# Kernel tuning notes

Measured on AMD Instinct MI355X. Metric: run time of the kernel, lower is better.

The kernel has to match this reference:

```python
import jax, jax.numpy as jnp
import numpy as np

B, T, NA, H, C = 64, 128, 2048, 1024, 10  # batch, time, n_act, hidden_units, classes
FORGET_BIAS = 1.0  # tf BasicLSTMCell default


def setup_inputs() -> dict:
    key = jax.random.key(0)
    ks = jax.random.split(key, 5)
    s = 0.02
    return {
        "inputs": jax.random.normal(ks[0], (B, T, NA), jnp.float32),
        "W0": jax.random.normal(ks[1], (NA + H, 4 * H), jnp.float32) * s,
        "b0": jnp.zeros((4 * H,), jnp.float32),
        "W1": jax.random.normal(ks[2], (2 * H, 4 * H), jnp.float32) * s,
        "b1": jnp.zeros((4 * H,), jnp.float32),
        "Wout": jax.random.normal(ks[3], (H, C), jnp.float32) * s,
        "bout": jnp.zeros((C,), jnp.float32),
    }


def _lstm_step(c, h, x, W, b):
    # tf.contrib.rnn.BasicLSTMCell: z = [x; h] @ W + b, gates order i, j, f, o
    z = jnp.concatenate([x, h], axis=-1) @ W + b
    i, j, f, o = jnp.split(z, 4, axis=-1)
    c_new = c * jax.nn.sigmoid(f + FORGET_BIAS) + jax.nn.sigmoid(i) * jnp.tanh(j)
    h_new = jnp.tanh(c_new) * jax.nn.sigmoid(o)
    return c_new, h_new


def reference(inputs, W0, b0, W1, b1, Wout, bout):
    Bz = inputs.shape[0]
    Hd = Wout.shape[0]

    def step(carry, x_t):
        c0, h0, c1, h1 = carry
        c0, h0 = _lstm_step(c0, h0, x_t, W0, b0)   # layer 0
        c1, h1 = _lstm_step(c1, h1, h0, W1, b1)    # layer 1
        return (c0, h0, c1, h1), h1

    z = jnp.zeros((Bz, Hd), inputs.dtype)
    init = (z, z, z, z)  # zero_state for both layers
    xs = jnp.swapaxes(inputs, 0, 1)  # [T, B, NA]
    _, hs = jax.lax.scan(step, init, xs)  # hs: [T, B, H]
    hs = jnp.swapaxes(hs, 0, 1)  # [B, T, H]
    logits = hs @ Wout + bout  # xw_plus_b on flattened outputs
    preds = jax.nn.softmax(logits, axis=-1)  # [B, T, C]
    return preds
```

## Files before the change

kernel.cpp:

```cpp
#include <hip/hip_runtime.h>
#include <stdint.h>


typedef __attribute__((ext_vector_type(4))) float f32x4;
typedef __attribute__((ext_vector_type(8))) short short8x;
typedef unsigned short ushort_t;

constexpr int B_  = 64;
constexpr int T_  = 128;
constexpr int NA_ = 2048;
constexpr int H_  = 1024;
constexpr int C_  = 10;
constexpr int BT_ = B_ * T_;
constexpr int G4_ = 4 * H_;
constexpr int HB_ = B_ * H_;
constexpr int CH_ = 32;
constexpr int MC_ = B_ * CH_;
constexpr int NWG_ = 256;

__device__ __forceinline__ ushort_t f2bf(float x) {
    uint32_t u = __float_as_uint(x);
    uint32_t r = (u + 0x7FFFu + ((u >> 16) & 1u)) >> 16;
    return (ushort_t)r;
}
__device__ __forceinline__ float bf2f(ushort_t h) {
    return __uint_as_float((uint32_t)h << 16);
}
__device__ __forceinline__ float sigmf(float x) { return 1.0f / (1.0f + expf(-x)); }

__device__ __forceinline__ void st_u32(void* p, uint32_t v) {
    __hip_atomic_store((uint32_t*)p, v, __ATOMIC_RELAXED, __HIP_MEMORY_SCOPE_AGENT);
}
__device__ __forceinline__ void st_u64(void* p, uint64_t v) {
    __hip_atomic_store((uint64_t*)p, v, __ATOMIC_RELAXED, __HIP_MEMORY_SCOPE_AGENT);
}

#define AH_ISSUE(dst, ptr) \
    asm volatile("global_load_dwordx4 %0, %1, off sc0 sc1" : "=v"(dst) : "v"(ptr))

#define GLOAD_LDS(gp, lp) \
    __builtin_amdgcn_global_load_lds((const __attribute__((address_space(1))) uint32_t*)(gp), \
                                     (__attribute__((address_space(3))) uint32_t*)(lp), 16, 0, 0)

__global__ void decomp_chunk(const float* __restrict__ X, int c,
                             ushort_t* __restrict__ Hi, ushort_t* __restrict__ Lo) {
    const int i = blockIdx.x * blockDim.x + threadIdx.x;
    if (i >= MC_ * NA_ / 4) return;
    const int mp = i >> 9;
    const int kq = i & 511;
    const int b = mp >> 5, j = mp & 31;
    const size_t src = ((size_t)(b * T_ + c * CH_ + j)) * NA_ + (size_t)kq * 4;
    float4 v = *(const float4*)(X + src);
    ushort4 hi, lo;
    hi.x = f2bf(v.x); lo.x = f2bf(v.x - bf2f(hi.x));
    hi.y = f2bf(v.y); lo.y = f2bf(v.y - bf2f(hi.y));
    hi.z = f2bf(v.z); lo.z = f2bf(v.z - bf2f(hi.z));
    hi.w = f2bf(v.w); lo.w = f2bf(v.w - bf2f(hi.w));
    ((ushort4*)Hi)[i] = hi;
    ((ushort4*)Lo)[i] = lo;
}

__global__ void transdec(const float* __restrict__ W, int rowOff, int Klen,
                         ushort_t* __restrict__ Thi, ushort_t* __restrict__ Tlo,
                         int swz) {
    __shared__ float tile[32][33];
    const int k0 = blockIdx.x * 32, n0 = blockIdx.y * 32;
    const int tx = threadIdx.x & 31, ty = threadIdx.x >> 5;
#pragma unroll
    for (int i = 0; i < 32; i += 8)
        tile[ty + i][tx] = W[(size_t)(rowOff + k0 + ty + i) * G4_ + n0 + tx];
    __syncthreads();
#pragma unroll
    for (int i = 0; i < 32; i += 8) {
        float v = tile[tx][ty + i];
        int n = n0 + ty + i;
        int kk = k0 + tx;
        ushort_t hi = f2bf(v);
        Thi[(size_t)n * Klen + kk] = hi;
        int kl = swz ? (kk ^ ((n & 7) << 3)) : kk;
        Tlo[(size_t)n * Klen + kl] = f2bf(v - bf2f(hi));
    }
}

__global__ __launch_bounds__(256, 2)
void gemm_bf16x3(const ushort_t* __restrict__ Ahi, const ushort_t* __restrict__ Alo,
                 const ushort_t* __restrict__ Bhi, const ushort_t* __restrict__ Blo,
                 float* __restrict__ C, int M, int N, int K) {
    __shared__ ushort_t sA[2][128 * 64];
    __shared__ ushort_t sB[2][128 * 64];

    const int tid  = threadIdx.x;
    const int lane = tid & 63;
    const int wv   = tid >> 6;
    const int wr   = wv >> 1, wc = wv & 1;
    const int tiles_n = N >> 7;
    int id = blockIdx.x;
    const int q8 = gridDim.x >> 3;
    id = (id & 7) * q8 + (id >> 3);
    const int tm = (id / tiles_n) * 128, tn = (id % tiles_n) * 128;

    f32x4 acc[4][4] = {};

    for (int k0 = 0; k0 < K; k0 += 64) {
#pragma unroll
        for (int rd = 0; rd < 4; ++rd) {
            const int off = rd * 4096 + tid * 16;
            const int r   = off >> 7;
            const int kc  = ((off >> 4) & 7) ^ (r & 7);
            const size_t aoff = (size_t)(tm + r) * K + k0 + kc * 8;
            const size_t boff = (size_t)(tn + r) * K + k0 + kc * 8;
            const int dst = (rd * 4096 + wv * 1024) >> 1;
            GLOAD_LDS(Ahi + aoff, (ushort_t*)sA[0] + dst);
            GLOAD_LDS(Alo + aoff, (ushort_t*)sA[1] + dst);
            GLOAD_LDS(Bhi + boff, (ushort_t*)sB[0] + dst);
            GLOAD_LDS(Blo + boff, (ushort_t*)sB[1] + dst);
        }
        __syncthreads();
#pragma unroll
        for (int ks = 0; ks < 2; ++ks) {
            short8x ah[4], al[4], bh[4], bl[4];
#pragma unroll
            for (int i = 0; i < 4; ++i) {
                const int kc = ks * 4 + (lane >> 4);
                const int ra = wr * 64 + i * 16 + (lane & 15);
                const int ea = ra * 64 + ((kc ^ (ra & 7)) * 8);
                ah[i] = *(const short8x*)(&sA[0][ea]);
                al[i] = *(const short8x*)(&sA[1][ea]);
                const int rb = wc * 64 + i * 16 + (lane & 15);
                const int eb = rb * 64 + ((kc ^ (rb & 7)) * 8);
                bh[i] = *(const short8x*)(&sB[0][eb]);
                bl[i] = *(const short8x*)(&sB[1][eb]);
            }
#pragma unroll
            for (int i = 0; i < 4; ++i)
#pragma unroll
                for (int j = 0; j < 4; ++j) {
                    acc[i][j] = __builtin_amdgcn_mfma_f32_16x16x32_bf16(ah[i], bh[j], acc[i][j], 0, 0, 0);
                    acc[i][j] = __builtin_amdgcn_mfma_f32_16x16x32_bf16(ah[i], bl[j], acc[i][j], 0, 0, 0);
                    acc[i][j] = __builtin_amdgcn_mfma_f32_16x16x32_bf16(al[i], bh[j], acc[i][j], 0, 0, 0);
                }
        }
        __syncthreads();
    }
#pragma unroll
    for (int i = 0; i < 4; ++i)
#pragma unroll
        for (int j = 0; j < 4; ++j)
#pragma unroll
            for (int qq = 0; qq < 4; ++qq) {
                const int row = tm + wr * 64 + i * 16 + (lane >> 4) * 4 + qq;
                const int col = tn + wc * 64 + j * 16 + (lane & 15);
                C[(size_t)row * N + col] = acc[i][j][qq];
            }
}

__device__ __forceinline__ void grid_bar(unsigned* slots, unsigned* flag, unsigned epoch) {
    __syncthreads();
    if (threadIdx.x == 0)
        __hip_atomic_store(&slots[blockIdx.x], epoch, __ATOMIC_RELAXED, __HIP_MEMORY_SCOPE_AGENT);
    if (blockIdx.x == 0) {
        if (threadIdx.x < NWG_) {
            unsigned spins = 0;
            while (__hip_atomic_load(&slots[threadIdx.x], __ATOMIC_RELAXED, __HIP_MEMORY_SCOPE_AGENT) < epoch
                   && ++spins < (1u << 20))
                __builtin_amdgcn_s_sleep(4);
        }
        __syncthreads();
        if (threadIdx.x == 0)
            __hip_atomic_store(flag, epoch, __ATOMIC_RELAXED, __HIP_MEMORY_SCOPE_AGENT);
    } else {
        if (threadIdx.x == 0) {
            unsigned spins = 0;
            while (__hip_atomic_load(flag, __ATOMIC_RELAXED, __HIP_MEMORY_SCOPE_AGENT) < epoch
                   && ++spins < (1u << 20))
                __builtin_amdgcn_s_sleep(4);
        }
    }
    __syncthreads();
}

__global__ __launch_bounds__(512, 1)
void lstm_persist(int t0, int t1,
                  const float* __restrict__ Z0c,
                  const ushort_t* __restrict__ W0hT_hi, const ushort_t* __restrict__ W0hT_lo,
                  const ushort_t* __restrict__ W1T_hi,  const ushort_t* __restrict__ W1T_lo,
                  const float* __restrict__ b0, const float* __restrict__ b1,
                  ushort_t* __restrict__ h0hi, ushort_t* __restrict__ h1hi,
                  float* __restrict__ c0, float* __restrict__ c1,
                  ushort_t* __restrict__ hs, unsigned* slots, unsigned* flag) {
    const int w = blockIdx.x;
    const bool isL0 = (w < 128);
    const int u0 = (isL0 ? w : w - 128) * 8;
    const int tid = threadIdx.x, lane = tid & 63, kv = tid >> 6;
    const int K   = isL0 ? H_ : 2 * H_;
    const int KS  = K >> 3;
    const int NKS = KS >> 5;
    const int kbase = kv * KS;

    __shared__ ushort_t slo[32 * 2048];
    __shared__ float zbuf[64][33];

    const ushort_t* Whi = isL0 ? W0hT_hi : W1T_hi;
    const ushort_t* Wlo = isL0 ? W0hT_lo : W1T_lo;

    const int nis = K >> 9;
    for (int g = 0; g < 4; ++g)
        for (int is = 0; is < nis; ++is) {
            const size_t selem = (size_t)(g * H_ + u0) * K + is * 4096 + kv * 512 + (size_t)lane * 8;
            ushort_t* dst = slo + g * 8 * K + is * 4096 + kv * 512;
            GLOAD_LDS(Wlo + selem, dst);
        }
    short8x wh[2][8] = {};
#pragma unroll
    for (int jn = 0; jn < 2; ++jn)
#pragma unroll
        for (int s = 0; s < 8; ++s)
            if (s < NKS) {
                const int n = jn * 16 + (lane & 15);
                const int grow = (n >> 3) * H_ + u0 + (n & 7);
                wh[jn][s] = *(const short8x*)(Whi + (size_t)grow * K + kbase + s * 32 + (lane >> 4) * 8);
            }
    __syncthreads();

    const bool epi = (tid < 256);
    const int em = tid >> 2;
    const int jp = (tid & 3) * 2;
    const int eu = u0 + jp;
    const float* bias = isL0 ? b0 : b1;
    const float bi0 = epi ? bias[eu]            : 0.f, bi1 = epi ? bias[eu + 1]            : 0.f;
    const float bj0 = epi ? bias[H_ + eu]       : 0.f, bj1 = epi ? bias[H_ + eu + 1]       : 0.f;
    const float bf0 = epi ? bias[2 * H_ + eu]   : 0.f, bf1 = epi ? bias[2 * H_ + eu + 1]   : 0.f;
    const float bo0 = epi ? bias[3 * H_ + eu]   : 0.f, bo1 = epi ? bias[3 * H_ + eu + 1]   : 0.f;
    const int zm = tid >> 3, zj = tid & 7;

    for (int t = t0; t < t1; ++t) {
        const bool active = isL0 ? (t < T_) : (t >= 1);
        if (active) {
            const int tt = isL0 ? t : t - 1;
            const ushort_t* Ah;
            int ka0;
            if (isL0)          { Ah = h0hi + ((tt + 1) & 1) * HB_; ka0 = kbase; }
            else if (kv < 4)   { Ah = h0hi + (tt & 1) * HB_;       ka0 = kbase; }
            else               { Ah = h1hi + ((tt + 1) & 1) * HB_; ka0 = kbase - H_; }

            zbuf[zm][zj] = 0.f; zbuf[zm][8 + zj] = 0.f;
            zbuf[zm][16 + zj] = 0.f; zbuf[zm][24 + zj] = 0.f;
            __syncthreads();

            float2 zx0 = {0.f, 0.f}, zx1 = {0.f, 0.f}, zx2 = {0.f, 0.f}, zx3 = {0.f, 0.f};
            if (isL0 && epi) {
                const float* zr = Z0c + ((size_t)em * CH_ + (tt & (CH_ - 1))) * G4_;
                zx0 = *(const float2*)(zr + eu);
                zx1 = *(const float2*)(zr + H_ + eu);
                zx2 = *(const float2*)(zr + 2 * H_ + eu);
                zx3 = *(const float2*)(zr + 3 * H_ + eu);
            }

            f32x4 acc[4][2] = {};
            short8x ah[2][4];
            const int npass = NKS >> 1;
#pragma unroll
            for (int pp = 0; pp < 4; ++pp)
                if (pp < npass) {
#pragma unroll
                    for (int s2 = 0; s2 < 2; ++s2) {
                        const int s = pp * 2 + s2;
                        const int kaa = ka0 + s * 32 + (lane >> 4) * 8;
#pragma unroll
                        for (int i = 0; i < 4; ++i)
                            AH_ISSUE(ah[s2][i], Ah + (size_t)(i * 16 + (lane & 15)) * H_ + kaa);
                    }
                    asm volatile("s_waitcnt vmcnt(0)" ::: "memory");
                    __builtin_amdgcn_sched_barrier(0);
#pragma unroll
                    for (int s2 = 0; s2 < 2; ++s2) {
                        const int s = pp * 2 + s2;
                        const int kw = kbase + s * 32 + (lane >> 4) * 8;
                        const int n0_ = (lane & 15);
                        short8x bl0 = *(const short8x*)(&slo[n0_ * K + (kw ^ ((n0_ & 7) << 3))]);
                        const int n1_ = 16 + (lane & 15);
                        short8x bl1 = *(const short8x*)(&slo[n1_ * K + (kw ^ ((n1_ & 7) << 3))]);
#pragma unroll
                        for (int i = 0; i < 4; ++i) {
                            acc[i][0] = __builtin_amdgcn_mfma_f32_16x16x32_bf16(ah[s2][i], wh[0][s], acc[i][0], 0, 0, 0);
                            acc[i][1] = __builtin_amdgcn_mfma_f32_16x16x32_bf16(ah[s2][i], wh[1][s], acc[i][1], 0, 0, 0);
                            acc[i][0] = __builtin_amdgcn_mfma_f32_16x16x32_bf16(ah[s2][i], bl0, acc[i][0], 0, 0, 0);
                            acc[i][1] = __builtin_amdgcn_mfma_f32_16x16x32_bf16(ah[s2][i], bl1, acc[i][1], 0, 0, 0);
                        }
                    }
                }
#pragma unroll
            for (int i2 = 0; i2 < 4; ++i2) {
                const int i = (i2 + (kv & 3)) & 3;
#pragma unroll
                for (int jn2 = 0; jn2 < 2; ++jn2) {
                    const int jn = (jn2 + (kv >> 2)) & 1;
#pragma unroll
                    for (int qq = 0; qq < 4; ++qq) {
                        const int m = i * 16 + (lane >> 4) * 4 + qq;
                        const int n = jn * 16 + (lane & 15);
                        atomicAdd(&zbuf[m][n], acc[i][jn][qq]);
                    }
                }
            }
            __syncthreads();

            if (epi) {
                const float zi0 = zbuf[em][jp]          + bi0 + zx0.x;
                const float zi1 = zbuf[em][jp + 1]      + bi1 + zx0.y;
                const float zj0 = zbuf[em][8 + jp]      + bj0 + zx1.x;
                const float zj1 = zbuf[em][8 + jp + 1]  + bj1 + zx1.y;
                const float zf0 = zbuf[em][16 + jp]     + bf0 + zx2.x;
                const float zf1 = zbuf[em][16 + jp + 1] + bf1 + zx2.y;
                const float zo0 = zbuf[em][24 + jp]     + bo0 + zx3.x;
                const float zo1 = zbuf[em][24 + jp + 1] + bo1 + zx3.y;
                const size_t sidx = (size_t)em * H_ + eu;
                float* cp = (isL0 ? c0 : c1) + sidx;
                const float cn0 = cp[0] * sigmf(zf0 + 1.0f) + sigmf(zi0) * tanhf(zj0);
                const float cn1 = cp[1] * sigmf(zf1 + 1.0f) + sigmf(zi1) * tanhf(zj1);
                union { float f[2]; uint64_t u; } cu;
                cu.f[0] = cn0; cu.f[1] = cn1;
                st_u64(cp, cu.u);
                const float hv0 = tanhf(cn0) * sigmf(zo0);
                const float hv1 = tanhf(cn1) * sigmf(zo1);
                const uint32_t hhp = (uint32_t)f2bf(hv0) | ((uint32_t)f2bf(hv1) << 16);
                if (isL0) {
                    st_u32(h0hi + (tt & 1) * HB_ + sidx, hhp);
                } else {
                    st_u32(h1hi + (tt & 1) * HB_ + sidx, hhp);
                    st_u32(hs + ((size_t)em * T_ + tt) * H_ + eu, hhp);
                }
            }
        }
        if (t < T_) grid_bar(slots, flag, (unsigned)(t + 1));
    }
}

__global__ __launch_bounds__(256)
void out_softmax(const ushort_t* __restrict__ hs, const float* __restrict__ Wout,
                 const float* __restrict__ bout, float* __restrict__ out) {
    const int row  = blockIdx.x * 4 + (threadIdx.x >> 6);
    const int lane = threadIdx.x & 63;
    const ushort_t* h = hs + (size_t)row * H_;
    float s[C_];
#pragma unroll
    for (int c = 0; c < C_; ++c) s[c] = 0.f;
    for (int k = lane; k < H_; k += 64) {
        const float hv = bf2f(h[k]);
        const float* w = Wout + k * C_;
#pragma unroll
        for (int c = 0; c < C_; ++c) s[c] += hv * w[c];
    }
#pragma unroll
    for (int c = 0; c < C_; ++c) {
#pragma unroll
        for (int d = 32; d > 0; d >>= 1) s[c] += __shfl_xor(s[c], d);
        s[c] += bout[c];
    }
    float mx = s[0];
#pragma unroll
    for (int c = 1; c < C_; ++c) mx = fmaxf(mx, s[c]);
    float sum = 0.f;
#pragma unroll
    for (int c = 0; c < C_; ++c) { s[c] = expf(s[c] - mx); sum += s[c]; }
    const float inv = 1.0f / sum;
    if (lane < C_) {
        float pv = 0.f;
#pragma unroll
        for (int c = 0; c < C_; ++c)
            if (lane == c) pv = s[c] * inv;
        out[(size_t)row * C_ + lane] = pv;
    }
}

extern "C" void kernel_launch(void* const* d_in, const int* in_sizes, int n_in,
                              void* d_out, int out_size, void* d_ws, size_t ws_size,
                              hipStream_t stream) {
    const float* X    = (const float*)d_in[0];
    const float* W0   = (const float*)d_in[1];
    const float* b0   = (const float*)d_in[2];
    const float* W1   = (const float*)d_in[3];
    const float* b1   = (const float*)d_in[4];
    const float* Wout = (const float*)d_in[5];
    const float* bout = (const float*)d_in[6];
    float* out = (float*)d_out;

    char* p = (char*)d_ws;
    size_t off = 0;
    auto take = [&](size_t bytes) { char* r = p + off; off += bytes; return r; };
    ushort_t* W0xT_hi = (ushort_t*)take((size_t)G4_ * NA_ * 2);
    ushort_t* W0xT_lo = (ushort_t*)take((size_t)G4_ * NA_ * 2);
    ushort_t* W0hT_hi = (ushort_t*)take((size_t)G4_ * H_ * 2);
    ushort_t* W0hT_lo = (ushort_t*)take((size_t)G4_ * H_ * 2);
    ushort_t* W1T_hi  = (ushort_t*)take((size_t)G4_ * 2 * H_ * 2);
    ushort_t* W1T_lo  = (ushort_t*)take((size_t)G4_ * 2 * H_ * 2);
    ushort_t* Xc_hi   = (ushort_t*)take((size_t)MC_ * NA_ * 2);
    ushort_t* Xc_lo   = (ushort_t*)take((size_t)MC_ * NA_ * 2);
    float*    Z0c     = (float*)take((size_t)MC_ * G4_ * 4);
    ushort_t* hsb     = (ushort_t*)take((size_t)BT_ * H_ * 2);
    float*    c0      = (float*)take((size_t)B_ * H_ * 4);
    float*    c1      = (float*)take((size_t)B_ * H_ * 4);
    ushort_t* h0hi    = (ushort_t*)take((size_t)2 * HB_ * 2);
    ushort_t* h1hi    = (ushort_t*)take((size_t)2 * HB_ * 2);
    unsigned* bar     = (unsigned*)take(2048);
    if (ws_size < off) return;

    unsigned* slots = bar;
    unsigned* flag  = bar + 256;

    (void)hipMemsetAsync(c0, 0, (size_t)B_ * H_ * 4, stream);
    (void)hipMemsetAsync(c1, 0, (size_t)B_ * H_ * 4, stream);
    (void)hipMemsetAsync(h0hi + HB_, 0, (size_t)HB_ * 2, stream);
    (void)hipMemsetAsync(h1hi + HB_, 0, (size_t)HB_ * 2, stream);
    (void)hipMemsetAsync(bar, 0, 2048, stream);

    transdec<<<dim3(NA_ / 32, G4_ / 32), 256, 0, stream>>>(W0, 0,   NA_,     W0xT_hi, W0xT_lo, 0);
    transdec<<<dim3(H_  / 32, G4_ / 32), 256, 0, stream>>>(W0, NA_, H_,      W0hT_hi, W0hT_lo, 1);
    transdec<<<dim3(2 * H_ / 32, G4_ / 32), 256, 0, stream>>>(W1, 0, 2 * H_, W1T_hi,  W1T_lo, 1);

    for (int c = 0; c < T_ / CH_; ++c) {
        decomp_chunk<<<(MC_ * NA_ / 4 + 255) / 256, 256, 0, stream>>>(X, c, Xc_hi, Xc_lo);
        gemm_bf16x3<<<(MC_ / 128) * (G4_ / 128), 256, 0, stream>>>(
            Xc_hi, Xc_lo, W0xT_hi, W0xT_lo, Z0c, MC_, G4_, NA_);
        lstm_persist<<<NWG_, 512, 0, stream>>>(c * CH_, c * CH_ + CH_, Z0c,
                                               W0hT_hi, W0hT_lo, W1T_hi, W1T_lo,
                                               b0, b1, h0hi, h1hi,
                                               c0, c1, hsb, slots, flag);
    }
    lstm_persist<<<NWG_, 512, 0, stream>>>(T_, T_ + 1, Z0c,
                                           W0hT_hi, W0hT_lo, W1T_hi, W1T_lo,
                                           b0, b1, h0hi, h1hi,
                                           c0, c1, hsb, slots, flag);

    out_softmax<<<BT_ / 4, 256, 0, stream>>>(hsb, Wout, bout, out);
}
```

Measured before the change: 4.673 ms.

## Block hidden-state layout by 8-unit groups and keep cell state in registers

Hidden-state buffers and the hs output now use a blocked layout of [unit-block][batch][8]. Each workgroup writes one contiguous 1 KB block, and the MFMA A-operand loads read contiguous 16-byte rows across the batch, which should improve coalescing for the per-step global reads that cross the grid barrier. The LSTM cell state is kept in registers for the whole persistent chunk and written back only once at the end, removing a global load and store per step. The output softmax kernel is updated to read the new strided layout, which may make its accesses less contiguous.

```diff
diff --git a/kernel.cpp b/kernel.cpp
--- a/kernel.cpp
+++ b/kernel.cpp
@@ -30,9 +30,6 @@
 
 __device__ __forceinline__ void st_u32(void* p, uint32_t v) {
     __hip_atomic_store((uint32_t*)p, v, __ATOMIC_RELAXED, __HIP_MEMORY_SCOPE_AGENT);
-}
-__device__ __forceinline__ void st_u64(void* p, uint64_t v) {
-    __hip_atomic_store((uint64_t*)p, v, __ATOMIC_RELAXED, __HIP_MEMORY_SCOPE_AGENT);
 }
 
 #define AH_ISSUE(dst, ptr) \
@@ -185,12 +182,13 @@
                   const ushort_t* __restrict__ W0hT_hi, const ushort_t* __restrict__ W0hT_lo,
                   const ushort_t* __restrict__ W1T_hi,  const ushort_t* __restrict__ W1T_lo,
                   const float* __restrict__ b0, const float* __restrict__ b1,
-                  ushort_t* __restrict__ h0hi, ushort_t* __restrict__ h1hi,
+                  ushort_t* __restrict__ h0blk, ushort_t* __restrict__ h1blk,
                   float* __restrict__ c0, float* __restrict__ c1,
-                  ushort_t* __restrict__ hs, unsigned* slots, unsigned* flag) {
+                  ushort_t* __restrict__ hsblk, unsigned* slots, unsigned* flag) {
     const int w = blockIdx.x;
     const bool isL0 = (w < 128);
-    const int u0 = (isL0 ? w : w - 128) * 8;
+    const int uB = isL0 ? w : (w - 128);
+    const int u0 = uB * 8;
     const int tid = threadIdx.x, lane = tid & 63, kv = tid >> 6;
     const int K   = isL0 ? H_ : 2 * H_;
     const int KS  = K >> 3;
@@ -233,15 +231,19 @@
     const float bo0 = epi ? bias[3 * H_ + eu]   : 0.f, bo1 = epi ? bias[3 * H_ + eu + 1]   : 0.f;
     const int zm = tid >> 3, zj = tid & 7;
 
+    float cr0 = 0.f, cr1 = 0.f;
+    float* cptr = (isL0 ? c0 : c1) + (size_t)em * H_ + eu;
+    if (epi) { float2 cv = *(const float2*)cptr; cr0 = cv.x; cr1 = cv.y; }
+
     for (int t = t0; t < t1; ++t) {
         const bool active = isL0 ? (t < T_) : (t >= 1);
         if (active) {
             const int tt = isL0 ? t : t - 1;
             const ushort_t* Ah;
             int ka0;
-            if (isL0)          { Ah = h0hi + ((tt + 1) & 1) * HB_; ka0 = kbase; }
-            else if (kv < 4)   { Ah = h0hi + (tt & 1) * HB_;       ka0 = kbase; }
-            else               { Ah = h1hi + ((tt + 1) & 1) * HB_; ka0 = kbase - H_; }
+            if (isL0)          { Ah = h0blk + ((tt + 1) & 1) * HB_; ka0 = kbase; }
+            else if (kv < 4)   { Ah = h0blk + (tt & 1) * HB_;       ka0 = kbase; }
+            else               { Ah = h1blk + ((tt + 1) & 1) * HB_; ka0 = kbase - H_; }
 
             zbuf[zm][zj] = 0.f; zbuf[zm][8 + zj] = 0.f;
             zbuf[zm][16 + zj] = 0.f; zbuf[zm][24 + zj] = 0.f;
@@ -267,8 +269,10 @@
                         const int s = pp * 2 + s2;
                         const int kaa = ka0 + s * 32 + (lane >> 4) * 8;
 #pragma unroll
-                        for (int i = 0; i < 4; ++i)
-                            AH_ISSUE(ah[s2][i], Ah + (size_t)(i * 16 + (lane & 15)) * H_ + kaa);
+                        for (int i = 0; i < 4; ++i) {
+                            const int batch = i * 16 + (lane & 15);
+                            AH_ISSUE(ah[s2][i], Ah + (size_t)(kaa >> 3) * 512 + (size_t)batch * 8);
+                        }
                     }
                     asm volatile("s_waitcnt vmcnt(0)" ::: "memory");
                     __builtin_amdgcn_sched_barrier(0);
@@ -314,26 +318,25 @@
                 const float zf1 = zbuf[em][16 + jp + 1] + bf1 + zx2.y;
                 const float zo0 = zbuf[em][24 + jp]     + bo0 + zx3.x;
                 const float zo1 = zbuf[em][24 + jp + 1] + bo1 + zx3.y;
-                const size_t sidx = (size_t)em * H_ + eu;
-                float* cp = (isL0 ? c0 : c1) + sidx;
-                const float cn0 = cp[0] * sigmf(zf0 + 1.0f) + sigmf(zi0) * tanhf(zj0);
-                const float cn1 = cp[1] * sigmf(zf1 + 1.0f) + sigmf(zi1) * tanhf(zj1);
-                union { float f[2]; uint64_t u; } cu;
-                cu.f[0] = cn0; cu.f[1] = cn1;
-                st_u64(cp, cu.u);
+                const float cn0 = cr0 * sigmf(zf0 + 1.0f) + sigmf(zi0) * tanhf(zj0);
+                const float cn1 = cr1 * sigmf(zf1 + 1.0f) + sigmf(zi1) * tanhf(zj1);
+                cr0 = cn0; cr1 = cn1;
                 const float hv0 = tanhf(cn0) * sigmf(zo0);
                 const float hv1 = tanhf(cn1) * sigmf(zo1);
                 const uint32_t hhp = (uint32_t)f2bf(hv0) | ((uint32_t)f2bf(hv1) << 16);
+                const size_t hoff = (size_t)uB * 512 + (size_t)em * 8 + jp;
                 if (isL0) {
-                    st_u32(h0hi + (tt & 1) * HB_ + sidx, hhp);
+                    st_u32(h0blk + (tt & 1) * HB_ + hoff, hhp);
                 } else {
-                    st_u32(h1hi + (tt & 1) * HB_ + sidx, hhp);
-                    st_u32(hs + ((size_t)em * T_ + tt) * H_ + eu, hhp);
+                    st_u32(h1blk + (tt & 1) * HB_ + hoff, hhp);
+                    st_u32(hsblk + ((size_t)tt * 128 + uB) * 512 + (size_t)em * 8 + jp, hhp);
                 }
             }
         }
         if (t < T_) grid_bar(slots, flag, (unsigned)(t + 1));
     }
+
+    if (epi) { float2 cv; cv.x = cr0; cv.y = cr1; *(float2*)cptr = cv; }
 }
 
 __global__ __launch_bounds__(256)
@@ -341,12 +344,12 @@
                  const float* __restrict__ bout, float* __restrict__ out) {
     const int row  = blockIdx.x * 4 + (threadIdx.x >> 6);
     const int lane = threadIdx.x & 63;
-    const ushort_t* h = hs + (size_t)row * H_;
+    const int b = row >> 7, t = row & (T_ - 1);
     float s[C_];
 #pragma unroll
     for (int c = 0; c < C_; ++c) s[c] = 0.f;
     for (int k = lane; k < H_; k += 64) {
-        const float hv = bf2f(h[k]);
+        const float hv = bf2f(hs[((size_t)t * 128 + (k >> 3)) * 512 + (size_t)b * 8 + (k & 7)]);
         const float* w = Wout + k * C_;
 #pragma unroll
         for (int c = 0; c < C_; ++c) s[c] += hv * w[c];
@@ -397,11 +400,11 @@
     ushort_t* Xc_hi   = (ushort_t*)take((size_t)MC_ * NA_ * 2);
     ushort_t* Xc_lo   = (ushort_t*)take((size_t)MC_ * NA_ * 2);
     float*    Z0c     = (float*)take((size_t)MC_ * G4_ * 4);
-    ushort_t* hsb     = (ushort_t*)take((size_t)BT_ * H_ * 2);
+    ushort_t* hsblk   = (ushort_t*)take((size_t)BT_ * H_ * 2);
     float*    c0      = (float*)take((size_t)B_ * H_ * 4);
     float*    c1      = (float*)take((size_t)B_ * H_ * 4);
-    ushort_t* h0hi    = (ushort_t*)take((size_t)2 * HB_ * 2);
-    ushort_t* h1hi    = (ushort_t*)take((size_t)2 * HB_ * 2);
+    ushort_t* h0blk   = (ushort_t*)take((size_t)2 * HB_ * 2);
+    ushort_t* h1blk   = (ushort_t*)take((size_t)2 * HB_ * 2);
     unsigned* bar     = (unsigned*)take(2048);
     if (ws_size < off) return;
 
@@ -410,8 +413,8 @@
 
     (void)hipMemsetAsync(c0, 0, (size_t)B_ * H_ * 4, stream);
     (void)hipMemsetAsync(c1, 0, (size_t)B_ * H_ * 4, stream);
-    (void)hipMemsetAsync(h0hi + HB_, 0, (size_t)HB_ * 2, stream);
-    (void)hipMemsetAsync(h1hi + HB_, 0, (size_t)HB_ * 2, stream);
+    (void)hipMemsetAsync(h0blk + HB_, 0, (size_t)HB_ * 2, stream);
+    (void)hipMemsetAsync(h1blk + HB_, 0, (size_t)HB_ * 2, stream);
     (void)hipMemsetAsync(bar, 0, 2048, stream);
 
     transdec<<<dim3(NA_ / 32, G4_ / 32), 256, 0, stream>>>(W0, 0,   NA_,     W0xT_hi, W0xT_lo, 0);
@@ -424,13 +427,13 @@
             Xc_hi, Xc_lo, W0xT_hi, W0xT_lo, Z0c, MC_, G4_, NA_);
         lstm_persist<<<NWG_, 512, 0, stream>>>(c * CH_, c * CH_ + CH_, Z0c,
                                                W0hT_hi, W0hT_lo, W1T_hi, W1T_lo,
-                                               b0, b1, h0hi, h1hi,
-                                               c0, c1, hsb, slots, flag);
+                                               b0, b1, h0blk, h1blk,
+                                               c0, c1, hsblk, slots, flag);
     }
     lstm_persist<<<NWG_, 512, 0, stream>>>(T_, T_ + 1, Z0c,
                                            W0hT_hi, W0hT_lo, W1T_hi, W1T_lo,
-                                           b0, b1, h0hi, h1hi,
-                                           c0, c1, hsb, slots, flag);
-
-    out_softmax<<<BT_ / 4, 256, 0, stream>>>(hsb, Wout, bout, out);
-}
+                                           b0, b1, h0blk, h1blk,
+                                           c0, c1, hsblk, slots, flag);
+
+    out_softmax<<<BT_ / 4, 256, 0, stream>>>(hsblk, Wout, bout, out);
+}
```

Result: faster. 4.447 ms (-4.8%).
